# Kernel optimization log

Hardware: AMD Instinct MI355X
Metric: run time of the kernel (lower is better)

Reference implementation:

```python
import jax, jax.numpy as jnp
import numpy as np

C = 64
CK = C // 8  # query/key channels

def setup_inputs() -> dict:
    key = jax.random.key(0)
    ks = jax.random.split(key, 8)
    x = jax.random.normal(ks[0], (4, C, 16, 16, 16), dtype=jnp.float32)
    # 1x1x1 Conv3d weights collapse to [out_ch, in_ch] matrices
    wq = jax.random.normal(ks[1], (CK, C), dtype=jnp.float32) * (1.0 / np.sqrt(C))
    bq = jax.random.normal(ks[2], (CK,), dtype=jnp.float32) * 0.01
    wk = jax.random.normal(ks[3], (CK, C), dtype=jnp.float32) * (1.0 / np.sqrt(C))
    bk = jax.random.normal(ks[4], (CK,), dtype=jnp.float32) * 0.01
    wv = jax.random.normal(ks[5], (C, C), dtype=jnp.float32) * (1.0 / np.sqrt(C))
    bv = jax.random.normal(ks[6], (C,), dtype=jnp.float32) * 0.01
    gamma = jnp.ones((1,), dtype=jnp.float32) * 0.5  # nonzero so attention path affects output
    return {"x": x, "wq": wq, "bq": bq, "wk": wk, "bk": bk, "wv": wv, "bv": bv, "gamma": gamma}

def reference(x, wq, bq, wk, bk, wv, bv, gamma):
    B, Cc, D, H, W = x.shape
    N = D * H * W
    xf = x.reshape(B, Cc, N)  # [B, C, N]
    q = jnp.einsum('kc,bcn->bkn', wq, xf) + bq[None, :, None]  # [B, CK, N]
    k = jnp.einsum('kc,bcn->bkn', wk, xf) + bk[None, :, None]  # [B, CK, N]
    v = jnp.einsum('oc,bcn->bon', wv, xf) + bv[None, :, None]  # [B, C, N]
    # energy[b,i,j] = sum_k q[b,k,i] * k[b,k,j]; softmax over j (no scaling, per source)
    energy = jnp.einsum('bki,bkj->bij', q, k)  # [B, N, N]
    attn = jax.nn.softmax(energy, axis=-1)
    # out[b,c,i] = sum_j v[b,c,j] * attn[b,i,j]
    out = jnp.einsum('bcj,bij->bci', v, attn)  # [B, C, N]
    out = out.reshape(B, Cc, D, H, W)
    return gamma * out + x
```

## Files before the change

kernel.cpp:

```cpp
#include <hip/hip_runtime.h>
#include <hip/hip_bf16.h>

#define BATCH  4
#define CDIM   64
#define CKD    8
#define NPOS   4096
#define RLN2   1.44269504f
#define SH2    25.96851039f
#define ECL2   14.42695041f
#define PTP    72

typedef _Float16 f16x8 __attribute__((ext_vector_type(8)));
typedef float    f32x4 __attribute__((ext_vector_type(4)));

__device__ __forceinline__ f16x8 pack8(const float* e) {
    f16x8 v;
#pragma unroll
    for (int i = 0; i < 8; ++i) v[i] = (_Float16)e[i];
    return v;
}

__device__ __forceinline__ void gl_lds16(const void* g, void* l) {
    __builtin_amdgcn_global_load_lds(
        (const __attribute__((address_space(1))) void*)g,
        (__attribute__((address_space(3))) void*)l, 16, 0, 0);
}
__device__ __forceinline__ void gl_lds4(const void* g, void* l) {
    __builtin_amdgcn_global_load_lds(
        (const __attribute__((address_space(1))) void*)g,
        (__attribute__((address_space(3))) void*)l, 4, 0, 0);
}

__global__ __launch_bounds__(256, 4) void proj_kernel(
    const float* __restrict__ x,
    const float* __restrict__ wq, const float* __restrict__ bq,
    const float* __restrict__ wk, const float* __restrict__ bk,
    const float* __restrict__ wv, const float* __restrict__ bv,
    _Float16* __restrict__ qh, _Float16* __restrict__ kh,
    _Float16* __restrict__ vswz)
{
    __shared__ float red[64 * 73];

    const int bid  = blockIdx.x;
    const int part = bid >> 8;
    const int tid  = threadIdx.x;
    const int s    = tid & 63;
    const int h    = __builtin_amdgcn_readfirstlane(tid >> 6);
    const int pos  = (bid & 255) * 64 + s;
    const int b    = pos >> 12;
    const int n    = pos & 4095;
    const int c0   = part * 16;
    const int cl0  = h * 16;

    const float* xb = x + (size_t)b * CDIM * NPOS + n;

    float vacc[16];
#pragma unroll
    for (int o = 0; o < 16; ++o) vacc[o] = 0.f;
    float qacc[8] = {0.f, 0.f, 0.f, 0.f, 0.f, 0.f, 0.f, 0.f};

    if (part < 2) {
        const float* wqk = (part == 0) ? wq : wk;
#pragma unroll
        for (int cc = 0; cc < 16; ++cc) {
            const int c = cl0 + cc;
            const float xv = xb[(size_t)c * NPOS];
#pragma unroll
            for (int o = 0; o < 8; ++o)  qacc[o] = fmaf(wqk[o * CDIM + c], xv, qacc[o]);
#pragma unroll
            for (int o = 0; o < 16; ++o) vacc[o] = fmaf(wv[(c0 + o) * CDIM + c], xv, vacc[o]);
        }
    } else {
#pragma unroll
        for (int cc = 0; cc < 16; ++cc) {
            const int c = cl0 + cc;
            const float xv = xb[(size_t)c * NPOS];
#pragma unroll
            for (int o = 0; o < 16; ++o) vacc[o] = fmaf(wv[(c0 + o) * CDIM + c], xv, vacc[o]);
        }
    }

    float* rs = red + s * 73;
    if (h != 0) {
        float* rh = rs + (h - 1) * 24;
        if (part < 2) {
#pragma unroll
            for (int i = 0; i < 8; ++i)  rh[i] = qacc[i];
#pragma unroll
            for (int o = 0; o < 16; ++o) rh[8 + o] = vacc[o];
        } else {
#pragma unroll
            for (int o = 0; o < 16; ++o) rh[o] = vacc[o];
        }
    }
    __syncthreads();
    if (h != 0) return;

    if (part < 2) {
#pragma unroll
        for (int i = 0; i < 8; ++i)  qacc[i] += rs[i] + rs[24 + i] + rs[48 + i];
#pragma unroll
        for (int o = 0; o < 16; ++o) vacc[o] += rs[8 + o] + rs[32 + o] + rs[56 + o];

        const float* bqk = (part == 0) ? bq : bk;
        const float scl  = (part == 0) ? RLN2 : 1.0f;
        f16x8 qv;
#pragma unroll
        for (int o = 0; o < 8; ++o) qv[o] = (_Float16)((qacc[o] + bqk[o]) * scl);
        _Float16* dst = ((part == 0) ? qh : kh) + ((size_t)(b * NPOS + n)) * CKD;
        *(f16x8*)dst = qv;
    } else {
#pragma unroll
        for (int o = 0; o < 16; ++o) vacc[o] += rs[o] + rs[24 + o] + rs[48 + o];
    }

    const int jq = (n >> 2) & 3;
    const int ju = ((n >> 4) & 1) * 4 + (n & 3);
    const size_t vbase = (size_t)(b * 128 + (n >> 5)) * 2048
                       + (size_t)part * 512 + jq * 128 + ju;
#pragma unroll
    for (int o = 0; o < 16; ++o)
        vswz[vbase + o * 8] = (_Float16)(vacc[o] + bv[c0 + o]);
}

template<int NSPLIT>
__global__ __launch_bounds__(256, 4) void attn_kernel(
    const _Float16* __restrict__ qh, const _Float16* __restrict__ kh,
    const _Float16* __restrict__ vswz,
    __hip_bfloat16* __restrict__ po, float* __restrict__ pl)
{
    constexpr int JCHUNK = NPOS / NSPLIT;
    constexpr int NIT64  = JCHUNK / 64;

    __shared__ __align__(16) _Float16 vbuf[3][4096];
    __shared__ __align__(16) _Float16 kbuf[3][512];
    __shared__ __hip_bfloat16 pt[4][16][PTP];

    const int bid   = blockIdx.x;
    const int split = bid & (NSPLIT - 1);
    const int itile = (bid / NSPLIT) & 31;
    const int b     = bid / (NSPLIT * 32);
    const int tid   = threadIdx.x;
    const int wave  = tid >> 6;
    const int lane  = tid & 63;
    const int quad  = lane >> 4;
    const int m16   = lane & 15;

    const int i0 = itile * 128 + wave * 32;

    f16x8 qa0 = *(const f16x8*)(qh + ((size_t)(b * NPOS + i0 + m16)) * CKD);
    f16x8 qa1 = *(const f16x8*)(qh + ((size_t)(b * NPOS + i0 + 16 + m16)) * CKD);
    if (quad != 0) { qa0 = (f16x8){}; qa1 = (f16x8){}; }

    const _Float16* vsrc = vswz + (size_t)b * 262144
                         + (size_t)split * (JCHUNK / 32) * 2048
                         + wave * 1024 + lane * 8;
    const _Float16* ksrc = kh + ((size_t)(b * NPOS + split * JCHUNK)) * CKD
                         + wave * 128 + lane * 2;

    f32x4 acc0[4], acc1[4];
#pragma unroll
    for (int nb = 0; nb < 4; ++nb) {
        acc0[nb] = (f32x4){0.f, 0.f, 0.f, 0.f};
        acc1[nb] = (f32x4){0.f, 0.f, 0.f, 0.f};
    }
    float ls0 = 0.f, ls1 = 0.f;
    const f32x4 csh = {-SH2, -SH2, -SH2, -SH2};

    gl_lds16(vsrc,              &vbuf[0][wave * 1024]);
    gl_lds16(vsrc + 512,        &vbuf[0][wave * 1024 + 512]);
    gl_lds4 (ksrc,              &kbuf[0][wave * 128]);
    gl_lds16(vsrc + 4096,       &vbuf[1][wave * 1024]);
    gl_lds16(vsrc + 4096 + 512, &vbuf[1][wave * 1024 + 512]);
    gl_lds4 (ksrc + 512,        &kbuf[1][wave * 128]);

    int cur = 0;
    for (int it = 0; it < NIT64; ++it) {
        asm volatile("s_waitcnt vmcnt(3)" ::: "memory");
        __builtin_amdgcn_s_barrier();

        const int nx2 = (cur == 0) ? 2 : cur - 1;
        {
            const _Float16* vn = vsrc + (size_t)(it + 2) * 4096;
            gl_lds16(vn,       &vbuf[nx2][wave * 1024]);
            gl_lds16(vn + 512, &vbuf[nx2][wave * 1024 + 512]);
            gl_lds4(ksrc + (size_t)(it + 2) * 512, &kbuf[nx2][wave * 128]);
        }

        const _Float16* kb = &kbuf[cur][0];
        const _Float16* vb0 = &vbuf[cur][0];

#pragma unroll
        for (int h = 0; h < 2; ++h) {
            const f16x8 kfa = *(const f16x8*)(kb + h * 256 + m16 * 8);
            const f16x8 kfb = *(const f16x8*)(kb + h * 256 + 128 + m16 * 8);

            __builtin_amdgcn_s_setprio(1);
            const f32x4 s0a = __builtin_amdgcn_mfma_f32_16x16x32_f16(kfa, qa0, csh, 0, 0, 0);
            const f32x4 s0b = __builtin_amdgcn_mfma_f32_16x16x32_f16(kfb, qa0, csh, 0, 0, 0);
            const f32x4 s1a = __builtin_amdgcn_mfma_f32_16x16x32_f16(kfa, qa1, csh, 0, 0, 0);
            const f32x4 s1b = __builtin_amdgcn_mfma_f32_16x16x32_f16(kfb, qa1, csh, 0, 0, 0);
            __builtin_amdgcn_s_setprio(0);

            float e0[8], e1[8];
#pragma unroll
            for (int r = 0; r < 4; ++r) {
                e0[r]     = __builtin_exp2f(fminf(s0a[r], ECL2));
                e0[4 + r] = __builtin_exp2f(fminf(s0b[r], ECL2));
                e1[r]     = __builtin_exp2f(fminf(s1a[r], ECL2));
                e1[4 + r] = __builtin_exp2f(fminf(s1b[r], ECL2));
            }
            ls0 += ((e0[0] + e0[1]) + (e0[2] + e0[3])) + ((e0[4] + e0[5]) + (e0[6] + e0[7]));
            ls1 += ((e1[0] + e1[1]) + (e1[2] + e1[3])) + ((e1[4] + e1[5]) + (e1[6] + e1[7]));

            const f16x8 pa0 = pack8(e0);
            const f16x8 pa1 = pack8(e1);

            __builtin_amdgcn_s_setprio(1);
#pragma unroll
            for (int nb = 0; nb < 4; ++nb) {
                const f16x8 vb = *(const f16x8*)(vb0 + h * 2048 + nb * 512 + quad * 128 + m16 * 8);
                acc0[nb] = __builtin_amdgcn_mfma_f32_16x16x32_f16(pa0, vb, acc0[nb], 0, 0, 0);
                acc1[nb] = __builtin_amdgcn_mfma_f32_16x16x32_f16(pa1, vb, acc1[nb], 0, 0, 0);
            }
            __builtin_amdgcn_s_setprio(0);
        }
        cur = (cur == 2) ? 0 : cur + 1;
    }

    ls0 += __shfl_xor(ls0, 16);
    ls0 += __shfl_xor(ls0, 32);
    ls1 += __shfl_xor(ls1, 16);
    ls1 += __shfl_xor(ls1, 32);

    const int sbx = split * BATCH + b;
    if (quad == 0) {
        pl[(size_t)sbx * NPOS + i0 + m16]      = ls0;
        pl[(size_t)sbx * NPOS + i0 + 16 + m16] = ls1;
    }

    __hip_bfloat16* ept = &pt[wave][0][0];

#define EPILOG(ACC, IOFS)                                                     \
    do {                                                                      \
        _Pragma("unroll")                                                     \
        for (int nb = 0; nb < 4; ++nb)                                        \
            _Pragma("unroll")                                                 \
            for (int r = 0; r < 4; ++r)                                       \
                ept[(quad * 4 + r) * PTP + nb * 16 + m16] =                   \
                    __float2bfloat16(ACC[nb][r]);                             \
        _Pragma("unroll")                                                     \
        for (int g2 = 0; g2 < 16; ++g2) {                                     \
            const int c = quad + g2 * 4;                                      \
            po[((size_t)sbx * CDIM + c) * NPOS + i0 + (IOFS) + m16] =         \
                ept[m16 * PTP + c];                                           \
        }                                                                     \
    } while (0)

    EPILOG(acc0, 0);
    EPILOG(acc1, 16);
#undef EPILOG
}

template<int NSPLIT>
__global__ __launch_bounds__(256) void combine_kernel(
    const float* __restrict__ x,
    const __hip_bfloat16* __restrict__ po, const float* __restrict__ pl,
    const float* __restrict__ gamma, float* __restrict__ out)
{
    const int t  = blockIdx.x * 256 + threadIdx.x;
    const int i4 = (t & 1023) * 4;
    const int c  = (t >> 10) & 63;
    const int b  = t >> 16;

    const unsigned short* pou = (const unsigned short*)po;

    float L0 = 0.f, L1 = 0.f, L2 = 0.f, L3 = 0.f;
    float O0 = 0.f, O1 = 0.f, O2 = 0.f, O3 = 0.f;
#pragma unroll
    for (int s = 0; s < NSPLIT; ++s) {
        const size_t sb = (size_t)(s * BATCH + b);
        const float4 lv = *(const float4*)(pl + sb * NPOS + i4);
        const ushort4 pv = *(const ushort4*)(pou + (sb * CDIM + c) * NPOS + i4);
        L0 += lv.x; L1 += lv.y; L2 += lv.z; L3 += lv.w;
        O0 += __uint_as_float((unsigned)pv.x << 16);
        O1 += __uint_as_float((unsigned)pv.y << 16);
        O2 += __uint_as_float((unsigned)pv.z << 16);
        O3 += __uint_as_float((unsigned)pv.w << 16);
    }
    const float g = gamma[0];
    const size_t xi = ((size_t)(b * CDIM + c)) * NPOS + i4;
    const float4 xv = *(const float4*)(x + xi);
    float4 o;
    o.x = fmaf(g, O0 / L0, xv.x);
    o.y = fmaf(g, O1 / L1, xv.y);
    o.z = fmaf(g, O2 / L2, xv.z);
    o.w = fmaf(g, O3 / L3, xv.w);
    *(float4*)(out + xi) = o;
}

extern "C" void kernel_launch(void* const* d_in, const int* in_sizes, int n_in,
                              void* d_out, int out_size, void* d_ws, size_t ws_size,
                              hipStream_t stream)
{
    const float* x     = (const float*)d_in[0];
    const float* wq    = (const float*)d_in[1];
    const float* bq    = (const float*)d_in[2];
    const float* wk    = (const float*)d_in[3];
    const float* bk    = (const float*)d_in[4];
    const float* wv    = (const float*)d_in[5];
    const float* bv    = (const float*)d_in[6];
    const float* gamma = (const float*)d_in[7];
    float* out = (float*)d_out;

    char* ws = (char*)d_ws;
    _Float16*       qh   = (_Float16*)(ws);
    _Float16*       kh   = (_Float16*)(ws + (256 << 10));
    _Float16*       vswz = (_Float16*)(ws + (512 << 10));
    __hip_bfloat16* po   = (__hip_bfloat16*)(ws + (2560 << 10));

    const size_t po8_end = (2560ull << 10) + 8ull * 4 * CDIM * NPOS * 2;
    const size_t need8   = po8_end + 8ull * 4 * NPOS * 4;

    proj_kernel<<<1024, 256, 0, stream>>>(x, wq, bq, wk, bk, wv, bv, qh, kh, vswz);

    if (ws_size >= need8) {
        float* pl = (float*)(ws + po8_end);
        attn_kernel<8><<<BATCH * 32 * 8, 256, 0, stream>>>(qh, kh, vswz, po, pl);
        combine_kernel<8><<<1024, 256, 0, stream>>>(x, po, pl, gamma, out);
    } else {
        const size_t po4_end = (2560ull << 10) + 4ull * 4 * CDIM * NPOS * 2;
        float* pl = (float*)(ws + po4_end);
        attn_kernel<4><<<BATCH * 32 * 4, 256, 0, stream>>>(qh, kh, vswz, po, pl);
        combine_kernel<4><<<1024, 256, 0, stream>>>(x, po, pl, gamma, out);
    }
}
```

Before: 114.8 us.

## Process 64 query rows per wave and raise key split count to 16

Each wave now covers 64 query rows (four 16-row groups) instead of 32. Every K and V fragment read from LDS therefore feeds twice as many MFMAs, which cuts LDS traffic per unit of work. To keep the same grid size, the key dimension is split 16 ways instead of 8, with a fallback to 8 when the workspace is too small. In exchange, each thread holds more accumulator registers, which risks spills under the 4-wave launch bound, and the partial-output traffic written and then read by the combine kernel doubles. The setprio hints are also dropped.

```diff
diff --git a/kernel.cpp b/kernel.cpp
--- a/kernel.cpp
+++ b/kernel.cpp
@@ -138,19 +138,24 @@
 
     const int bid   = blockIdx.x;
     const int split = bid & (NSPLIT - 1);
-    const int itile = (bid / NSPLIT) & 31;
-    const int b     = bid / (NSPLIT * 32);
+    const int itile = (bid / NSPLIT) & 15;
+    const int b     = bid / (NSPLIT * 16);
     const int tid   = threadIdx.x;
     const int wave  = tid >> 6;
     const int lane  = tid & 63;
     const int quad  = lane >> 4;
     const int m16   = lane & 15;
 
-    const int i0 = itile * 128 + wave * 32;
-
-    f16x8 qa0 = *(const f16x8*)(qh + ((size_t)(b * NPOS + i0 + m16)) * CKD);
-    f16x8 qa1 = *(const f16x8*)(qh + ((size_t)(b * NPOS + i0 + 16 + m16)) * CKD);
-    if (quad != 0) { qa0 = (f16x8){}; qa1 = (f16x8){}; }
+    const int i0 = itile * 256 + wave * 64;
+
+    f16x8 qa[4];
+#pragma unroll
+    for (int s = 0; s < 4; ++s)
+        qa[s] = *(const f16x8*)(qh + ((size_t)(b * NPOS + i0 + s * 16 + m16)) * CKD);
+    if (quad != 0) {
+#pragma unroll
+        for (int s = 0; s < 4; ++s) qa[s] = (f16x8){};
+    }
 
     const _Float16* vsrc = vswz + (size_t)b * 262144
                          + (size_t)split * (JCHUNK / 32) * 2048
@@ -158,13 +163,12 @@
     const _Float16* ksrc = kh + ((size_t)(b * NPOS + split * JCHUNK)) * CKD
                          + wave * 128 + lane * 2;
 
-    f32x4 acc0[4], acc1[4];
-#pragma unroll
-    for (int nb = 0; nb < 4; ++nb) {
-        acc0[nb] = (f32x4){0.f, 0.f, 0.f, 0.f};
-        acc1[nb] = (f32x4){0.f, 0.f, 0.f, 0.f};
-    }
-    float ls0 = 0.f, ls1 = 0.f;
+    f32x4 acc[4][4];
+#pragma unroll
+    for (int s = 0; s < 4; ++s)
+#pragma unroll
+        for (int nb = 0; nb < 4; ++nb) acc[s][nb] = (f32x4){0.f, 0.f, 0.f, 0.f};
+    float ls[4] = {0.f, 0.f, 0.f, 0.f};
     const f32x4 csh = {-SH2, -SH2, -SH2, -SH2};
 
     gl_lds16(vsrc,              &vbuf[0][wave * 1024]);
@@ -194,49 +198,44 @@
         for (int h = 0; h < 2; ++h) {
             const f16x8 kfa = *(const f16x8*)(kb + h * 256 + m16 * 8);
             const f16x8 kfb = *(const f16x8*)(kb + h * 256 + 128 + m16 * 8);
-
-            __builtin_amdgcn_s_setprio(1);
-            const f32x4 s0a = __builtin_amdgcn_mfma_f32_16x16x32_f16(kfa, qa0, csh, 0, 0, 0);
-            const f32x4 s0b = __builtin_amdgcn_mfma_f32_16x16x32_f16(kfb, qa0, csh, 0, 0, 0);
-            const f32x4 s1a = __builtin_amdgcn_mfma_f32_16x16x32_f16(kfa, qa1, csh, 0, 0, 0);
-            const f32x4 s1b = __builtin_amdgcn_mfma_f32_16x16x32_f16(kfb, qa1, csh, 0, 0, 0);
-            __builtin_amdgcn_s_setprio(0);
-
-            float e0[8], e1[8];
-#pragma unroll
-            for (int r = 0; r < 4; ++r) {
-                e0[r]     = __builtin_exp2f(fminf(s0a[r], ECL2));
-                e0[4 + r] = __builtin_exp2f(fminf(s0b[r], ECL2));
-                e1[r]     = __builtin_exp2f(fminf(s1a[r], ECL2));
-                e1[4 + r] = __builtin_exp2f(fminf(s1b[r], ECL2));
+            f16x8 vb[4];
+#pragma unroll
+            for (int nb = 0; nb < 4; ++nb)
+                vb[nb] = *(const f16x8*)(vb0 + h * 2048 + nb * 512 + quad * 128 + m16 * 8);
+
+#pragma unroll
+            for (int s = 0; s < 4; ++s) {
+                const f32x4 sa = __builtin_amdgcn_mfma_f32_16x16x32_f16(kfa, qa[s], csh, 0, 0, 0);
+                const f32x4 sb = __builtin_amdgcn_mfma_f32_16x16x32_f16(kfb, qa[s], csh, 0, 0, 0);
+
+                float e[8];
+#pragma unroll
+                for (int r = 0; r < 4; ++r) {
+                    e[r]     = __builtin_exp2f(fminf(sa[r], ECL2));
+                    e[4 + r] = __builtin_exp2f(fminf(sb[r], ECL2));
+                }
+                ls[s] += ((e[0] + e[1]) + (e[2] + e[3])) + ((e[4] + e[5]) + (e[6] + e[7]));
+
+                const f16x8 pa = pack8(e);
+#pragma unroll
+                for (int nb = 0; nb < 4; ++nb)
+                    acc[s][nb] = __builtin_amdgcn_mfma_f32_16x16x32_f16(pa, vb[nb], acc[s][nb], 0, 0, 0);
             }
-            ls0 += ((e0[0] + e0[1]) + (e0[2] + e0[3])) + ((e0[4] + e0[5]) + (e0[6] + e0[7]));
-            ls1 += ((e1[0] + e1[1]) + (e1[2] + e1[3])) + ((e1[4] + e1[5]) + (e1[6] + e1[7]));
-
-            const f16x8 pa0 = pack8(e0);
-            const f16x8 pa1 = pack8(e1);
-
-            __builtin_amdgcn_s_setprio(1);
-#pragma unroll
-            for (int nb = 0; nb < 4; ++nb) {
-                const f16x8 vb = *(const f16x8*)(vb0 + h * 2048 + nb * 512 + quad * 128 + m16 * 8);
-                acc0[nb] = __builtin_amdgcn_mfma_f32_16x16x32_f16(pa0, vb, acc0[nb], 0, 0, 0);
-                acc1[nb] = __builtin_amdgcn_mfma_f32_16x16x32_f16(pa1, vb, acc1[nb], 0, 0, 0);
-            }
-            __builtin_amdgcn_s_setprio(0);
         }
         cur = (cur == 2) ? 0 : cur + 1;
     }
 
-    ls0 += __shfl_xor(ls0, 16);
-    ls0 += __shfl_xor(ls0, 32);
-    ls1 += __shfl_xor(ls1, 16);
-    ls1 += __shfl_xor(ls1, 32);
+#pragma unroll
+    for (int s = 0; s < 4; ++s) {
+        ls[s] += __shfl_xor(ls[s], 16);
+        ls[s] += __shfl_xor(ls[s], 32);
+    }
 
     const int sbx = split * BATCH + b;
     if (quad == 0) {
-        pl[(size_t)sbx * NPOS + i0 + m16]      = ls0;
-        pl[(size_t)sbx * NPOS + i0 + 16 + m16] = ls1;
+#pragma unroll
+        for (int s = 0; s < 4; ++s)
+            pl[(size_t)sbx * NPOS + i0 + s * 16 + m16] = ls[s];
     }
 
     __hip_bfloat16* ept = &pt[wave][0][0];
@@ -257,8 +256,10 @@
         }                                                                     \
     } while (0)
 
-    EPILOG(acc0, 0);
-    EPILOG(acc1, 16);
+    EPILOG(acc[0], 0);
+    EPILOG(acc[1], 16);
+    EPILOG(acc[2], 32);
+    EPILOG(acc[3], 48);
 #undef EPILOG
 }
 
@@ -319,19 +320,20 @@
     _Float16*       vswz = (_Float16*)(ws + (512 << 10));
     __hip_bfloat16* po   = (__hip_bfloat16*)(ws + (2560 << 10));
 
-    const size_t po8_end = (2560ull << 10) + 8ull * 4 * CDIM * NPOS * 2;
-    const size_t need8   = po8_end + 8ull * 4 * NPOS * 4;
+    const size_t po16_end = (2560ull << 10) + 16ull * 4 * CDIM * NPOS * 2;
+    const size_t need16   = po16_end + 16ull * 4 * NPOS * 4;
+    const size_t po8_end  = (2560ull << 10) + 8ull * 4 * CDIM * NPOS * 2;
+    const size_t need8    = po8_end + 8ull * 4 * NPOS * 4;
 
     proj_kernel<<<1024, 256, 0, stream>>>(x, wq, bq, wk, bk, wv, bv, qh, kh, vswz);
 
-    if (ws_size >= need8) {
+    if (ws_size >= need16) {
+        float* pl = (float*)(ws + po16_end);
+        attn_kernel<16><<<BATCH * 16 * 16, 256, 0, stream>>>(qh, kh, vswz, po, pl);
+        combine_kernel<16><<<1024, 256, 0, stream>>>(x, po, pl, gamma, out);
+    } else {
         float* pl = (float*)(ws + po8_end);
-        attn_kernel<8><<<BATCH * 32 * 8, 256, 0, stream>>>(qh, kh, vswz, po, pl);
+        attn_kernel<8><<<BATCH * 16 * 8, 256, 0, stream>>>(qh, kh, vswz, po, pl);
         combine_kernel<8><<<1024, 256, 0, stream>>>(x, po, pl, gamma, out);
-    } else {
-        const size_t po4_end = (2560ull << 10) + 4ull * 4 * CDIM * NPOS * 2;
-        float* pl = (float*)(ws + po4_end);
-        attn_kernel<4><<<BATCH * 32 * 4, 256, 0, stream>>>(qh, kh, vswz, po, pl);
-        combine_kernel<4><<<1024, 256, 0, stream>>>(x, po, pl, gamma, out);
-    }
-}
+    }
+}
```

Result: slower. 189.3 us (+64.9%).
